# Kernel optimization log

Hardware: AMD Instinct MI355X
Metric: run time of the kernel (lower is better)

Reference implementation:

```python
import jax, jax.numpy as jnp
import numpy as np

BN_EPS = 1e-5


def setup_inputs() -> dict:
    key = jax.random.key(0)
    k1, k2, k3, k4, k5 = jax.random.split(key, 5)
    B, N, K, C_in, C_out = 8, 8192, 16, 64, 64
    x = jax.random.normal(k1, (B, N, C_in), dtype=jnp.float32)
    knn = jax.random.randint(k2, (B, N, K), 0, N, dtype=jnp.int64)
    # learned params: linear weight (out, in), BN affine params.
    # NOTE: module inits bn.weight to `init`=0.0 which would zero the output;
    # we use random gamma so the baseline exercises nontrivial math.
    W = jax.random.normal(k3, (C_out, C_in), dtype=jnp.float32) * (1.0 / np.sqrt(C_in))
    gamma = jax.random.normal(k4, (C_out,), dtype=jnp.float32) * 0.1 + 1.0
    beta = jax.random.normal(k5, (C_out,), dtype=jnp.float32) * 0.1
    return {"x": x, "knn": knn, "W": W, "gamma": gamma, "beta": beta}


def reference(x, knn, W, gamma, beta):
    B, N, C = x.shape
    # linear projection (no bias): [B,N,C_in] x [C_out,C_in] -> [B,N,C_out]
    h = jnp.einsum('bnc,oc->bno', x, W)
    # KNN gather + mean aggregation: agg[b,n] = mean_k h[b, knn[b,n,k]]
    agg = jax.vmap(lambda hb, kb: hb[kb])(h, knn).mean(axis=2)  # [B,N,C_out]
    # BatchNorm1d in training mode over B*N tokens (biased variance)
    flat = agg.reshape(B * N, -1)
    mu = flat.mean(axis=0)
    var = flat.var(axis=0)
    out = (flat - mu) * jax.lax.rsqrt(var + BN_EPS) * gamma + beta
    return out.reshape(B, N, -1)
```

## Files before the change

kernel.cpp:

```cpp
#include <hip/hip_runtime.h>

typedef float f4 __attribute__((ext_vector_type(4)));

#define BB 8
#define NN 8192
#define KK 16
#define CC 64
#define TPB 64
#define THREADS 256
#define NCHUNK 1024
#define NTOK (BB * NN)
#define BN_EPS 1e-5f

__global__ __launch_bounds__(THREADS, 4) void k_main(
    const float* __restrict__ x, const int* __restrict__ knn,
    const float* __restrict__ W, float* __restrict__ out,
    float* __restrict__ partials)
{
    __shared__ float sWt[CC][CC];
    __shared__ union { float agg[TPB][CC + 4]; float red[2][16][CC]; } u;

    const int tid   = threadIdx.x;
    const int batch = blockIdx.x & 7;
    const int nb    = (blockIdx.x >> 3) * TPB;

    for (int i = tid; i < CC * CC; i += THREADS)
        sWt[i & 63][i >> 6] = W[i];

    const int g = tid >> 4, l = tid & 15;
    const f4* __restrict__ x4b = (const f4*)x + (size_t)batch * NN * (CC / 4);

    for (int it = 0; it < 4; ++it) {
        const int t = it * 16 + g;
        const int idx_my =
            __builtin_nontemporal_load(&knn[(batch * NN + nb + t) * KK + l]);
        int idxs[16];
        #pragma unroll
        for (int k = 0; k < KK; ++k) idxs[k] = __shfl(idx_my, k, 16);
        f4 v[16];
        #pragma unroll
        for (int k = 0; k < KK; ++k) v[k] = x4b[idxs[k] * (CC / 4) + l];
        #pragma unroll
        for (int s = 8; s; s >>= 1)
            #pragma unroll
            for (int k = 0; k < s; ++k) v[k] += v[k + s];
        *(f4*)&u.agg[t][l * 4] = v[0] * (1.0f / KK);
    }
    __syncthreads();

    const int tq = tid >> 4, oq = tid & 15;
    float acc[4][4] = {};
    #pragma unroll
    for (int c4 = 0; c4 < CC; c4 += 4) {
        float av[4][4], wv[4][4];
        #pragma unroll
        for (int t = 0; t < 4; ++t) {
            const f4 tmp = *(const f4*)&u.agg[tq * 4 + t][c4];
            av[t][0] = tmp.x; av[t][1] = tmp.y; av[t][2] = tmp.z; av[t][3] = tmp.w;
        }
        #pragma unroll
        for (int cc = 0; cc < 4; ++cc) {
            const f4 tmp = *(const f4*)&sWt[c4 + cc][oq * 4];
            wv[cc][0] = tmp.x; wv[cc][1] = tmp.y; wv[cc][2] = tmp.z; wv[cc][3] = tmp.w;
        }
        #pragma unroll
        for (int t = 0; t < 4; ++t)
            #pragma unroll
            for (int cc = 0; cc < 4; ++cc)
                #pragma unroll
                for (int o = 0; o < 4; ++o)
                    acc[t][o] += av[t][cc] * wv[cc][o];
    }

    f4* __restrict__ out4 = (f4*)out;
    #pragma unroll
    for (int t = 0; t < 4; ++t) {
        f4 r; r.x = acc[t][0]; r.y = acc[t][1]; r.z = acc[t][2]; r.w = acc[t][3];
        __builtin_nontemporal_store(
            r, &out4[(size_t)(batch * NN + nb + tq * 4 + t) * (CC / 4) + oq]);
    }

    __syncthreads();
    float ps[4] = {}, pq[4] = {};
    #pragma unroll
    for (int t = 0; t < 4; ++t)
        #pragma unroll
        for (int o = 0; o < 4; ++o) {
            ps[o] += acc[t][o];
            pq[o] += acc[t][o] * acc[t][o];
        }
    #pragma unroll
    for (int o = 0; o < 4; ++o) {
        u.red[0][tq][oq * 4 + o] = ps[o];
        u.red[1][tq][oq * 4 + o] = pq[o];
    }
    __syncthreads();
    if (tid < 128) {
        const int w = tid >> 6, c = tid & 63;
        float s = 0.f;
        #pragma unroll
        for (int i = 0; i < 16; ++i) s += u.red[w][i][c];
        partials[(size_t)blockIdx.x * 128 + tid] = s;
    }
}

__global__ __launch_bounds__(THREADS) void k_stats(
    const float* __restrict__ partials, const float* __restrict__ gamma,
    const float* __restrict__ beta, float* __restrict__ ss)
{
    __shared__ float sFin[8];
    const int tid = threadIdx.x;
    const int j = blockIdx.x;
    float s1 = 0.f, s2 = 0.f;
    for (int i = tid; i < NCHUNK; i += THREADS) {
        s1 += partials[(size_t)i * 128 + j];
        s2 += partials[(size_t)i * 128 + 64 + j];
    }
    #pragma unroll
    for (int off = 32; off; off >>= 1) {
        s1 += __shfl_down(s1, off);
        s2 += __shfl_down(s2, off);
    }
    if ((tid & 63) == 0) { sFin[tid >> 6] = s1; sFin[4 + (tid >> 6)] = s2; }
    __syncthreads();
    if (tid == 0) {
        const float S1 = sFin[0] + sFin[1] + sFin[2] + sFin[3];
        const float S2 = sFin[4] + sFin[5] + sFin[6] + sFin[7];
        const float invn = 1.0f / (float)NTOK;
        const float mu  = S1 * invn;
        const float var = S2 * invn - mu * mu;
        const float sc  = gamma[j] * rsqrtf(var + BN_EPS);
        ss[j]      = sc;
        ss[CC + j] = beta[j] - mu * sc;
    }
}

__global__ __launch_bounds__(256) void k_norm(
    float* __restrict__ out, const float* __restrict__ ss)
{
    const int idx = blockIdx.x * 256 + threadIdx.x;
    f4* out4 = (f4*)out;
    const f4 a  = out4[idx];
    const int c4 = idx & (CC / 4 - 1);
    const f4 sc = ((const f4*)ss)[c4];
    const f4 sh = ((const f4*)ss)[CC / 4 + c4];
    f4 r;
    r.x = fmaf(a.x, sc.x, sh.x);
    r.y = fmaf(a.y, sc.y, sh.y);
    r.z = fmaf(a.z, sc.z, sh.z);
    r.w = fmaf(a.w, sc.w, sh.w);
    __builtin_nontemporal_store(r, &out4[idx]);
}

extern "C" void kernel_launch(void* const* d_in, const int* in_sizes, int n_in,
                              void* d_out, int out_size, void* d_ws, size_t ws_size,
                              hipStream_t stream)
{
    const float* x     = (const float*)d_in[0];
    const int*   knn   = (const int*)d_in[1];
    const float* W     = (const float*)d_in[2];
    const float* gamma = (const float*)d_in[3];
    const float* beta  = (const float*)d_in[4];
    float* out = (float*)d_out;

    float* partials = (float*)d_ws;
    float* ss       = partials + NCHUNK * 128;

    k_main <<<NCHUNK, THREADS, 0, stream>>>(x, knn, W, out, partials);
    k_stats<<<64, THREADS, 0, stream>>>(partials, gamma, beta, ss);
    k_norm <<<(NTOK * CC) / 4 / 256, 256, 0, stream>>>(out, ss);
}
```

Before: 40.74 us.

## Assign chunks to blocks by XCC id via atomic tickets for L2 locality

Each block reads its hardware XCC id and claims a chunk from a per-batch atomic ticket counter, preferring the batch matching its XCC. Each batch's gathered x rows then mostly stay within one XCC's L2 cache instead of being spread over all eight, aiming to raise L2 hit rates for the random KNN gathers. The cost is an extra memset launch, an atomic per block and a syncthreads before work starts. Work can also become unbalanced when some XCCs spill over into other batches.

```diff
diff --git a/kernel.cpp b/kernel.cpp
--- a/kernel.cpp
+++ b/kernel.cpp
@@ -8,24 +8,44 @@
 #define CC 64
 #define TPB 64
 #define THREADS 256
-#define NCHUNK 1024
+#define CPB (NN / TPB)
+#define NCHUNK (BB * CPB)
 #define NTOK (BB * NN)
 #define BN_EPS 1e-5f
 
 __global__ __launch_bounds__(THREADS, 4) void k_main(
     const float* __restrict__ x, const int* __restrict__ knn,
     const float* __restrict__ W, float* __restrict__ out,
-    float* __restrict__ partials)
+    float* __restrict__ partials, int* __restrict__ tickets)
 {
     __shared__ float sWt[CC][CC];
     __shared__ union { float agg[TPB][CC + 4]; float red[2][16][CC]; } u;
+    __shared__ int sChunk;
 
-    const int tid   = threadIdx.x;
-    const int batch = blockIdx.x & 7;
-    const int nb    = (blockIdx.x >> 3) * TPB;
+    const int tid = threadIdx.x;
 
+    if (tid == 0) {
+        unsigned int xcc;
+        asm volatile("s_getreg_b32 %0, hwreg(HW_REG_XCC_ID)" : "=s"(xcc));
+        xcc &= 7;
+        int got = -1;
+        #pragma unroll
+        for (int a = 0; a < 8; ++a) {
+            const int bb = (xcc + a) & 7;
+            if (got < 0) {
+                const int t = atomicAdd(&tickets[bb], 1);
+                if (t < CPB) got = bb * CPB + t;
+            }
+        }
+        sChunk = got;
+    }
     for (int i = tid; i < CC * CC; i += THREADS)
         sWt[i & 63][i >> 6] = W[i];
+    __syncthreads();
+
+    const int ch    = sChunk;
+    const int batch = ch >> 7;
+    const int nb    = (ch & (CPB - 1)) * TPB;
 
     const int g = tid >> 4, l = tid & 15;
     const f4* __restrict__ x4b = (const f4*)x + (size_t)batch * NN * (CC / 4);
@@ -100,7 +120,7 @@
         float s = 0.f;
         #pragma unroll
         for (int i = 0; i < 16; ++i) s += u.red[w][i][c];
-        partials[(size_t)blockIdx.x * 128 + tid] = s;
+        partials[(size_t)ch * 128 + tid] = s;
     }
 }
 
@@ -165,8 +185,10 @@
 
     float* partials = (float*)d_ws;
     float* ss       = partials + NCHUNK * 128;
+    int*   tickets  = (int*)(ss + 128);
 
-    k_main <<<NCHUNK, THREADS, 0, stream>>>(x, knn, W, out, partials);
+    hipMemsetAsync(tickets, 0, 8 * sizeof(int), stream);
+    k_main <<<NCHUNK, THREADS, 0, stream>>>(x, knn, W, out, partials, tickets);
     k_stats<<<64, THREADS, 0, stream>>>(partials, gamma, beta, ss);
     k_norm <<<(NTOK * CC) / 4 / 256, 256, 0, stream>>>(out, ss);
 }
```

New measurement: 58.83 us. 1.44x slower.

## Pretranspose W in separate kernel, stage knn in LDS, raise occupancy

Applied to the files above, without the earlier changes.

Adds a tiny kernel that transposes W once into workspace, so the main kernel reads W^T directly from global/L2 instead of staging a 16KB transposed copy in shared memory per block. The knn indices for the tile are now loaded into LDS with one coalesced int4 load per thread, replacing per-lane loads plus shuffles. With less LDS per block, the launch bound rises to 7 blocks per CU to increase occupancy and latency hiding for the gather. The trade-off is an extra kernel launch and W reads from cache in the inner GEMM loop instead of LDS.

```diff
diff --git a/kernel.cpp b/kernel.cpp
--- a/kernel.cpp
+++ b/kernel.cpp
@@ -12,34 +12,45 @@
 #define NTOK (BB * NN)
 #define BN_EPS 1e-5f
 
-__global__ __launch_bounds__(THREADS, 4) void k_main(
+__global__ __launch_bounds__(256) void k_wt(
+    const float* __restrict__ W, float* __restrict__ wt)
+{
+    const int i = blockIdx.x * 256 + threadIdx.x;
+    wt[i] = W[(i & 63) * 64 + (i >> 6)];
+}
+
+__global__ __launch_bounds__(THREADS, 7) void k_main(
     const float* __restrict__ x, const int* __restrict__ knn,
-    const float* __restrict__ W, float* __restrict__ out,
+    const float* __restrict__ wt, float* __restrict__ out,
     float* __restrict__ partials)
 {
-    __shared__ float sWt[CC][CC];
+    __shared__ int sKnn[TPB * KK];
     __shared__ union { float agg[TPB][CC + 4]; float red[2][16][CC]; } u;
 
     const int tid   = threadIdx.x;
     const int batch = blockIdx.x & 7;
     const int nb    = (blockIdx.x >> 3) * TPB;
 
-    for (int i = tid; i < CC * CC; i += THREADS)
-        sWt[i & 63][i >> 6] = W[i];
+    ((int4*)sKnn)[tid] =
+        ((const int4*)&knn[(size_t)(batch * NN + nb) * KK])[tid];
+    __syncthreads();
 
     const int g = tid >> 4, l = tid & 15;
     const f4* __restrict__ x4b = (const f4*)x + (size_t)batch * NN * (CC / 4);
 
     for (int it = 0; it < 4; ++it) {
         const int t = it * 16 + g;
-        const int idx_my =
-            __builtin_nontemporal_load(&knn[(batch * NN + nb + t) * KK + l]);
         int idxs[16];
         #pragma unroll
-        for (int k = 0; k < KK; ++k) idxs[k] = __shfl(idx_my, k, 16);
+        for (int q = 0; q < 4; ++q) {
+            const int4 ii = ((const int4*)sKnn)[t * 4 + q];
+            idxs[q * 4 + 0] = ii.x; idxs[q * 4 + 1] = ii.y;
+            idxs[q * 4 + 2] = ii.z; idxs[q * 4 + 3] = ii.w;
+        }
         f4 v[16];
         #pragma unroll
-        for (int k = 0; k < KK; ++k) v[k] = x4b[idxs[k] * (CC / 4) + l];
+        for (int k = 0; k < KK; ++k)
+            v[k] = x4b[(size_t)idxs[k] * (CC / 4) + l];
         #pragma unroll
         for (int s = 8; s; s >>= 1)
             #pragma unroll
@@ -49,6 +60,7 @@
     __syncthreads();
 
     const int tq = tid >> 4, oq = tid & 15;
+    const f4* __restrict__ wt4 = (const f4*)wt;
     float acc[4][4] = {};
     #pragma unroll
     for (int c4 = 0; c4 < CC; c4 += 4) {
@@ -60,7 +72,7 @@
         }
         #pragma unroll
         for (int cc = 0; cc < 4; ++cc) {
-            const f4 tmp = *(const f4*)&sWt[c4 + cc][oq * 4];
+            const f4 tmp = wt4[(c4 + cc) * 16 + oq];
             wv[cc][0] = tmp.x; wv[cc][1] = tmp.y; wv[cc][2] = tmp.z; wv[cc][3] = tmp.w;
         }
         #pragma unroll
@@ -165,8 +177,10 @@
 
     float* partials = (float*)d_ws;
     float* ss       = partials + NCHUNK * 128;
+    float* wt       = ss + 128;
 
-    k_main <<<NCHUNK, THREADS, 0, stream>>>(x, knn, W, out, partials);
+    k_wt   <<<CC * CC / 256, 256, 0, stream>>>(W, wt);
+    k_main <<<NCHUNK, THREADS, 0, stream>>>(x, knn, wt, out, partials);
     k_stats<<<64, THREADS, 0, stream>>>(partials, gamma, beta, ss);
     k_norm <<<(NTOK * CC) / 4 / 256, 256, 0, stream>>>(out, ss);
 }
```

Result: slower. 51.02 us (+25.2%).
